# Kernel tuning notes

Hardware: AMD Instinct MI355X
Metric: run time of the kernel (lower is better)

The kernel has to match this reference:

```python
import jax, jax.numpy as jnp
import numpy as np

NUM_CLASSES = 3
EXCEPT_THRESH = 0.05
NMS_THRESH = 0.5
NMS_TOPK = 500
BATCH = 16
ANCHORS_PER_LOC = 3


def _make_scale(key, grid, stride):
    """Build realistic YOLO-style output / anchor / offset / stride tensors for one scale."""
    A = ANCHORS_PER_LOC
    N = grid * grid * A
    out = jax.random.normal(key, (BATCH, N, 5 + NUM_CLASSES), dtype=jnp.float32)
    ys, xs = jnp.meshgrid(jnp.arange(grid, dtype=jnp.float32),
                          jnp.arange(grid, dtype=jnp.float32), indexing='ij')
    off = jnp.stack([xs, ys], axis=-1).reshape(grid * grid, 1, 2)         # (G*G,1,2)
    off = jnp.broadcast_to(off, (grid * grid, A, 2)).reshape(1, N, 2)
    base = jnp.array([[16., 16.], [32., 24.], [24., 48.]], jnp.float32) * (stride / 8.0)
    anc = jnp.broadcast_to(base.reshape(1, 1, A, 2), (1, grid * grid, A, 2)).reshape(1, N, 2)
    st = jnp.full((1, 1, 2), stride, dtype=jnp.float32)
    return out, anc, off, st


def setup_inputs() -> dict:
    key = jax.random.key(0)
    k1, k2, k3 = jax.random.split(key, 3)
    o1, a1, f1, s1 = _make_scale(k1, 96, 8.0)
    o2, a2, f2, s2 = _make_scale(k2, 48, 16.0)
    o3, a3, f3, s3 = _make_scale(k3, 24, 32.0)
    return {
        'output1': o1, 'output2': o2, 'output3': o3,
        'anchor1': a1, 'anchor2': a2, 'anchor3': a3,
        'offset1': f1, 'offset2': f2, 'offset3': f3,
        'stride1': s1, 'stride2': s2, 'stride3': s3,
    }


def _decode(out, anchor, offset, stride):
    """YOLOv3 multiperclass decode -> (B, N*C, 6) rows of [id, score, x1, y1, x2, y2]."""
    xy, wh = out[..., 0:2], out[..., 2:4]
    obj, cls = out[..., 4:5], out[..., 5:]
    # from_sigmoid=False: apply sigmoid to centers / objectness / class logits
    xy = jax.nn.sigmoid(xy)
    obj = jax.nn.sigmoid(obj)
    cls = jax.nn.sigmoid(cls)
    center = (xy + offset) * stride              # (B,N,2)
    half = 0.5 * jnp.exp(wh) * anchor            # (B,N,2)
    bbox = jnp.concatenate([center - half, center + half], axis=-1)  # (B,N,4)
    scores = obj * cls                           # (B,N,C)
    B, N, C = scores.shape
    ids = jnp.broadcast_to(jnp.arange(C, dtype=jnp.float32), (B, N, C))
    mask = scores > EXCEPT_THRESH
    ids = jnp.where(mask, ids, -1.0)
    scr = jnp.where(mask, scores, -1.0)
    bb = jnp.broadcast_to(bbox[:, :, None, :], (B, N, C, 4))
    res = jnp.concatenate([ids[..., None], scr[..., None], bb], axis=-1)
    return res.reshape(B, N * C, 6)


def _iou_matrix(boxes):
    """boxes (K,4) corner format -> (K,K) IoU."""
    x1, y1, x2, y2 = boxes[:, 0], boxes[:, 1], boxes[:, 2], boxes[:, 3]
    area = jnp.maximum(x2 - x1, 0.0) * jnp.maximum(y2 - y1, 0.0)
    iw = jnp.maximum(jnp.minimum(x2[:, None], x2[None]) - jnp.maximum(x1[:, None], x1[None]), 0.0)
    ih = jnp.maximum(jnp.minimum(y2[:, None], y2[None]) - jnp.maximum(y1[:, None], y1[None]), 0.0)
    inter = iw * ih
    return inter / (area[:, None] + area[None] - inter + 1e-12)


def _greedy_keep(iou, valid):
    """Greedy NMS over score-sorted candidates. iou (K,K), valid (K,) -> keep (K,) bool."""
    K = iou.shape[0]
    ar = jnp.arange(K)
    def body(i, keep):
        suppressed = jnp.any(keep & (ar < i) & (iou[i] > NMS_THRESH))
        return keep.at[i].set(valid[i] & ~suppressed)
    return jax.lax.fori_loop(0, K, body, valid)


def _per_class_nms(ids, scores, bboxes):
    """ids/scores (B,M,1), bboxes (B,M,4). Suppressed candidates get id=-1, score=-1.
    uid=-1 (background / below-threshold) entries pass through untouched, matching the
    original which skips NMS for uid<0."""
    B, M = ids.shape[:2]
    idf, scf = ids[..., 0], scores[..., 0]
    scatter = jax.vmap(lambda kf, o, k: kf.at[o].set(k))
    for c in range(NUM_CLASSES):
        cmask = idf == float(c)
        s = jnp.where(cmask, scf, -jnp.inf)
        order = jnp.argsort(-s, axis=1)[:, :NMS_TOPK]            # (B,K)
        sb = jnp.take_along_axis(s, order, axis=1)               # (B,K)
        bb = jnp.take_along_axis(bboxes, order[..., None], axis=1)  # (B,K,4)
        valid = jnp.isfinite(sb)
        iou = jax.vmap(_iou_matrix)(bb)                          # (B,K,K)
        keep = jax.vmap(_greedy_keep)(iou, valid)                # (B,K)
        keep_full = scatter(jnp.zeros((B, M), bool), order, keep)
        sup = cmask & ~keep_full                                 # suppressed or beyond topk
        idf = jnp.where(sup, -1.0, idf)
        scf = jnp.where(sup, -1.0, scf)
    return idf[..., None], scf[..., None], bboxes


def reference(output1, output2, output3, anchor1, anchor2, anchor3,
              offset1, offset2, offset3, stride1, stride2, stride3):
    results = jnp.concatenate([
        _decode(output1, anchor1, offset1, stride1),
        _decode(output2, anchor2, offset2, stride2),
        _decode(output3, anchor3, offset3, stride3),
    ], axis=1)                                   # (B, M, 6)
    ids = results[:, :, 0:1]
    scores = results[:, :, 1:2]
    bboxes = results[:, :, 2:]
    return _per_class_nms(ids, scores, bboxes)
```

## Files before the change

kernel.cpp:

```cpp
#include <hip/hip_runtime.h>

#define N1 27648
#define N2 6912
#define N3 1728
#define NTOT 36288
#define BATCH_ 16
#define C_ 3
#define GRP (BATCH_ * C_)
#define MROWS (NTOT * C_)
#define TOPK 500
#define NBINS 2304
#define CCAP 2048
#define BASEBITS 0x3D400000u
#define TPRE 0.5f
#define LISTCAP 4096
#define CNT_STRIDE 32

#define OFF_LIST   8192ull
#define SZ_LIST    ((size_t)GRP * LISTCAP * 8)
#define OFF_KEYS   (OFF_LIST + SZ_LIST)
#define SZ_KEYS    ((size_t)GRP * 512 * 8)
#define OFF_BOXES  (OFF_KEYS + SZ_KEYS)
#define SZ_BOXES   ((size_t)GRP * 512 * 16)
#define OFF_MASKS  (OFF_BOXES + SZ_BOXES)
#define SZ_MASKS   ((size_t)GRP * 4096 * 8)
#define OFF_KCNT   (OFF_MASKS + SZ_MASKS)
#define SZ_KCNT    4096ull
#define WS_NEED    (OFF_KCNT + SZ_KCNT)

__device__ __forceinline__ float sigm(float x) { return 1.0f / (1.0f + expf(-x)); }

__device__ __forceinline__ float score_of(int b, int n, int c,
    const float* __restrict__ o1, const float* __restrict__ o2, const float* __restrict__ o3)
{
    const float* o; int ln, Ns;
    if (n < N1)           { o = o1; ln = n;             Ns = N1; }
    else if (n < N1 + N2) { o = o2; ln = n - N1;        Ns = N2; }
    else                  { o = o3; ln = n - (N1 + N2); Ns = N3; }
    const float* r = o + ((size_t)b * Ns + ln) * 8;
    return sigm(r[4]) * sigm(r[5 + c]);
}

__device__ __forceinline__ unsigned wave_push(bool pred, unsigned* cntp)
{
    unsigned long long mb = __ballot(pred);
    unsigned pos = 0xFFFFFFFFu;
    if (pred) {
        int lane = threadIdx.x & 63;
        int leader = __ffsll((long long)mb) - 1;
        unsigned total = (unsigned)__popcll(mb);
        unsigned base = 0;
        if (lane == leader) base = atomicAdd(cntp, total);
        base = __shfl(base, leader);
        pos = base + (unsigned)__popcll(mb & ((1ull << lane) - 1ull));
    }
    return pos;
}

__device__ __forceinline__ void scan_tb(const unsigned* hist, unsigned* sh_tb)
{
    const int tid = threadIdx.x;
    if (tid < 64) {
        const int CHUNK = NBINS / 64;
        int base_i = tid * CHUNK;
        unsigned own = 0;
        #pragma unroll
        for (int k = 0; k < CHUNK; ++k) own += hist[base_i + k];
        unsigned sfx = own;
        #pragma unroll
        for (int off = 1; off < 64; off <<= 1) {
            unsigned v = __shfl_down(sfx, off, 64);
            sfx += (tid + off < 64) ? v : 0u;
        }
        unsigned sfxn = sfx - own;
        if (tid == 0 && sfx < TOPK) *sh_tb = 0u;
        if (sfx >= TOPK && sfxn < TOPK) {
            unsigned cum = sfxn, tb = (unsigned)base_i;
            for (int k = CHUNK - 1; k >= 0; --k) {
                cum += hist[base_i + k];
                if (cum >= TOPK) { tb = (unsigned)(base_i + k); break; }
            }
            *sh_tb = tb;
        }
    }
}

__global__ __launch_bounds__(64) void zerocnt_kernel(unsigned* __restrict__ cnts)
{
    if (threadIdx.x < GRP) cnts[threadIdx.x * CNT_STRIDE] = 0u;
}

__global__ __launch_bounds__(256) void decode_filter_kernel(
    const float* __restrict__ o1, const float* __restrict__ o2, const float* __restrict__ o3,
    const float* __restrict__ a1, const float* __restrict__ a2, const float* __restrict__ a3,
    const float* __restrict__ f1, const float* __restrict__ f2, const float* __restrict__ f3,
    const float* __restrict__ s1, const float* __restrict__ s2, const float* __restrict__ s3,
    float* __restrict__ out,
    unsigned* __restrict__ cnts, unsigned long long* __restrict__ list, int listcap)
{
    __shared__ unsigned lcnt[C_];
    __shared__ unsigned lbase[C_];
    __shared__ unsigned long long stage[C_][256];

    const int tid = threadIdx.x;
    const int n = blockIdx.x * 256 + tid;
    const int b = blockIdx.y;

    if (tid < C_) lcnt[tid] = 0u;
    __syncthreads();

    if (n < NTOT) {
        const float *o, *anc, *off, *st; int ln, Ns;
        if (n < N1)           { o = o1; anc = a1; off = f1; st = s1; ln = n;             Ns = N1; }
        else if (n < N1 + N2) { o = o2; anc = a2; off = f2; st = s2; ln = n - N1;        Ns = N2; }
        else                  { o = o3; anc = a3; off = f3; st = s3; ln = n - (N1 + N2); Ns = N3; }
        const float* r = o + ((size_t)b * Ns + ln) * 8;
        float4 v0 = *(const float4*)r;
        float4 v1 = *(const float4*)(r + 4);

        float sx = sigm(v0.x);
        float sy = sigm(v0.y);
        float cx = (sx + off[2 * ln + 0]) * st[0];
        float cy = (sy + off[2 * ln + 1]) * st[1];
        float hx = 0.5f * expf(v0.z) * anc[2 * ln + 0];
        float hy = 0.5f * expf(v0.w) * anc[2 * ln + 1];
        float4 bb = make_float4(cx - hx, cy - hy, cx + hx, cy + hy);

        size_t base = (size_t)b * MROWS + (size_t)n * C_;
        float* ids = out;
        float* scs = out + (size_t)BATCH_ * MROWS;
        float* bbs = out + 2ull * BATCH_ * MROWS;

        __builtin_nontemporal_store(-1.0f, &ids[base + 0]);
        __builtin_nontemporal_store(-1.0f, &ids[base + 1]);
        __builtin_nontemporal_store(-1.0f, &ids[base + 2]);
        __builtin_nontemporal_store(-1.0f, &scs[base + 0]);
        __builtin_nontemporal_store(-1.0f, &scs[base + 1]);
        __builtin_nontemporal_store(-1.0f, &scs[base + 2]);
        float4* bp = (float4*)(bbs + base * 4);
        bp[0] = bb; bp[1] = bb; bp[2] = bb;

        if (listcap > 0) {
            float sobj = sigm(v1.x);
            float s[3] = { sobj * sigm(v1.y), sobj * sigm(v1.z), sobj * sigm(v1.w) };
            #pragma unroll
            for (int c = 0; c < C_; ++c) {
                if (s[c] > TPRE) {
                    unsigned p = atomicAdd(&lcnt[c], 1u);
                    stage[c][p] =
                        ((unsigned long long)__float_as_uint(s[c]) << 32) | (unsigned)(~n);
                }
            }
        }
    }

    if (listcap > 0) {
        __syncthreads();
        if (tid < C_)
            lbase[tid] = atomicAdd(&cnts[(b * C_ + tid) * CNT_STRIDE], lcnt[tid]);
        __syncthreads();
        #pragma unroll
        for (int c = 0; c < C_; ++c) {
            unsigned m = lcnt[c];
            if ((unsigned)tid < m) {
                unsigned pos = lbase[c] + (unsigned)tid;
                if (pos < (unsigned)listcap)
                    list[(size_t)(b * C_ + c) * listcap + pos] = stage[c][tid];
            }
        }
    }
}

__global__ __launch_bounds__(512) void topk_kernel(
    const float* __restrict__ o1, const float* __restrict__ o2, const float* __restrict__ o3,
    const float* __restrict__ out,
    const unsigned* __restrict__ cnts, const unsigned long long* __restrict__ list,
    unsigned long long* __restrict__ gkeys, float4* __restrict__ gboxes,
    unsigned* __restrict__ kcnt)
{
    const int g = blockIdx.x;
    const int b = g / C_;
    const int c = g - b * C_;
    const int tid = threadIdx.x;

    __shared__ unsigned long long smem[CCAP + 1152];
    unsigned long long* keys = smem;
    unsigned* hist = (unsigned*)(smem + CCAP);
    unsigned long long* skeys = smem + CCAP;
    __shared__ unsigned int sh_tb, sh_cnt;

    unsigned cnt_g = cnts[g * CNT_STRIDE];
    const bool pathL = (cnt_g >= TOPK && cnt_g <= (unsigned)LISTCAP);
    const unsigned long long* L = list + (size_t)g * LISTCAP;

    for (int i = tid; i < NBINS; i += 512) hist[i] = 0u;
    if (tid == 0) sh_cnt = 0u;
    __syncthreads();

    if (pathL) {
        #pragma unroll 4
        for (unsigned i = tid; i < cnt_g; i += 512) {
            unsigned bin = ((unsigned)(L[i] >> 32) - BASEBITS) >> 14;
            if (bin > NBINS - 1u) bin = NBINS - 1u;
            atomicAdd(&hist[bin], 1u);
        }
    } else {
        for (int n = tid; n < NTOT; n += 512) {
            float s = score_of(b, n, c, o1, o2, o3);
            if (s > 0.05f) {
                unsigned bin = (__float_as_uint(s) - BASEBITS) >> 14;
                if (bin > NBINS - 1u) bin = NBINS - 1u;
                atomicAdd(&hist[bin], 1u);
            }
        }
    }
    __syncthreads();

    scan_tb(hist, &sh_tb);
    __syncthreads();

    const unsigned tb = sh_tb;
    if (pathL) {
        unsigned nIter = (cnt_g + 511u) & ~511u;
        #pragma unroll 4
        for (unsigned i = tid; i < nIter; i += 512) {
            bool pred = false; unsigned long long key = 0ull;
            if (i < cnt_g) {
                key = L[i];
                unsigned bin = ((unsigned)(key >> 32) - BASEBITS) >> 14;
                if (bin > NBINS - 1u) bin = NBINS - 1u;
                pred = (bin >= tb);
            }
            unsigned p = wave_push(pred, &sh_cnt);
            if (pred && p < CCAP) keys[p] = key;
        }
    } else {
        const int nIter = (NTOT + 511) & ~511;
        for (int n = tid; n < nIter; n += 512) {
            bool pred = false; unsigned long long key = 0ull;
            if (n < NTOT) {
                float s = score_of(b, n, c, o1, o2, o3);
                if (s > 0.05f) {
                    unsigned bits = __float_as_uint(s);
                    unsigned bin = (bits - BASEBITS) >> 14;
                    if (bin > NBINS - 1u) bin = NBINS - 1u;
                    if (bin >= tb) {
                        pred = true;
                        key = ((unsigned long long)bits << 32) | (unsigned)(~n);
                    }
                }
            }
            unsigned p = wave_push(pred, &sh_cnt);
            if (pred && p < CCAP) keys[p] = key;
        }
    }
    __syncthreads();

    const unsigned cnt2 = min(sh_cnt, (unsigned)CCAP);
    const int K = (int)min(cnt2, (unsigned)TOPK);

    for (unsigned m = tid; m < cnt2; m += 512) {
        unsigned long long km = keys[m];
        unsigned rank = 0;
        #pragma unroll 4
        for (unsigned j = 0; j < cnt2; ++j)
            rank += (keys[j] > km) ? 1u : 0u;
        if (rank < 512u) skeys[rank] = km;
    }
    __syncthreads();

    if (tid == 0) kcnt[g] = (unsigned)K;
    if (tid < K) {
        unsigned long long key = skeys[tid];
        gkeys[(size_t)g * 512 + tid] = key;
        unsigned idx = ~(unsigned)(key & 0xFFFFFFFFull);
        const float* bbs = out + 2ull * BATCH_ * MROWS;
        gboxes[(size_t)g * 512 + tid] =
            *(const float4*)(bbs + ((size_t)b * MROWS + (size_t)idx * C_) * 4);
    }
}

__global__ __launch_bounds__(256) void masks_kernel(
    const float4* __restrict__ gboxes, const unsigned* __restrict__ kcnt,
    unsigned long long* __restrict__ gmasks)
{
    const int g = blockIdx.x;
    const int w = blockIdx.y;
    const int K = (int)kcnt[g];

    __shared__ float bx[TOPK * 4];
    __shared__ float ar[TOPK];

    const float4* B = gboxes + (size_t)g * 512;
    for (int j = threadIdx.x; j < K; j += 256) {
        float4 v = B[j];
        bx[j*4+0] = v.x; bx[j*4+1] = v.y; bx[j*4+2] = v.z; bx[j*4+3] = v.w;
        ar[j] = fmaxf(v.z - v.x, 0.0f) * fmaxf(v.w - v.y, 0.0f);
    }
    __syncthreads();

    unsigned long long* M = gmasks + (size_t)g * 4096 + (size_t)w * 512;
    const int j0 = w * 64;
    const int jhi = (K < j0 + 64) ? K : j0 + 64;

    for (int i = threadIdx.x; i < K; i += 256) {
        unsigned long long word = 0ull;
        if (i + 1 < jhi) {
            float xi1 = bx[i*4+0], yi1 = bx[i*4+1], xi2 = bx[i*4+2], yi2 = bx[i*4+3];
            float ai = ar[i];
            for (int j = j0; j < jhi; ++j) {
                float xj1 = bx[j*4+0], yj1 = bx[j*4+1], xj2 = bx[j*4+2], yj2 = bx[j*4+3];
                float aj = ar[j];
                float iw = fmaxf(fminf(xi2, xj2) - fmaxf(xi1, xj1), 0.0f);
                float ih = fmaxf(fminf(yi2, yj2) - fmaxf(yi1, yj1), 0.0f);
                float inter = iw * ih;
                float iou = inter / (ai + aj - inter + 1e-12f);
                if (iou > 0.5f && j > i) word |= 1ull << (j - j0);
            }
        }
        M[i] = word;
    }
}

__global__ __launch_bounds__(512) void greedy_kernel(
    const unsigned long long* __restrict__ gmasks,
    const unsigned long long* __restrict__ gkeys,
    const unsigned* __restrict__ kcnt, float* __restrict__ out)
{
    const int g = blockIdx.x;
    const int b = g / C_;
    const int c = g - b * C_;
    const int tid = threadIdx.x;
    const int K = (int)kcnt[g];

    __shared__ unsigned long long mlds[512 * 9];
    __shared__ unsigned long long keep_s[8];

    const unsigned long long* GM = gmasks + (size_t)g * 4096;
    for (int t = tid; t < 8 * 512; t += 512) {
        int w = t >> 9, i = t & 511;
        mlds[i * 9 + w] = (i < K) ? GM[w * 512 + i] : 0ull;
    }
    __syncthreads();

    if (tid < 64) {
        const int lane8 = tid & 7;
        unsigned long long removed = 0ull, keep = 0ull;
        const int Kpad = (K + 7) & ~7;

        unsigned long long m0 = mlds[0*9+lane8], m1 = mlds[1*9+lane8],
                           m2 = mlds[2*9+lane8], m3 = mlds[3*9+lane8],
                           m4 = mlds[4*9+lane8], m5 = mlds[5*9+lane8],
                           m6 = mlds[6*9+lane8], m7 = mlds[7*9+lane8];

        for (int i0 = 0; i0 < Kpad; i0 += 8) {
            int nb = (i0 + 8 < 512) ? (i0 + 8) : 0;
            unsigned long long n0 = mlds[(nb+0)*9+lane8], n1 = mlds[(nb+1)*9+lane8],
                               n2 = mlds[(nb+2)*9+lane8], n3 = mlds[(nb+3)*9+lane8],
                               n4 = mlds[(nb+4)*9+lane8], n5 = mlds[(nb+5)*9+lane8],
                               n6 = mlds[(nb+6)*9+lane8], n7 = mlds[(nb+7)*9+lane8];

            #define GSTEP(t, mt) { \
                int i = i0 + t; \
                int w = i >> 6, bp = i & 63; \
                bool mine = (tid == w) && ((removed >> bp) & 1ull); \
                unsigned long long alive = __any(mine) ? 0ull : ~0ull; \
                keep |= ((tid == w) ? (1ull << bp) : 0ull) & alive; \
                removed |= mt & alive; \
            }
            GSTEP(0, m0) GSTEP(1, m1) GSTEP(2, m2) GSTEP(3, m3)
            GSTEP(4, m4) GSTEP(5, m5) GSTEP(6, m6) GSTEP(7, m7)
            #undef GSTEP

            m0=n0; m1=n1; m2=n2; m3=n3; m4=n4; m5=n5; m6=n6; m7=n7;
        }
        if (tid < 8) keep_s[tid] = keep;
    }
    __syncthreads();

    const unsigned long long* GK = gkeys + (size_t)g * 512;
    for (int i = tid; i < K; i += 512) {
        if ((keep_s[i >> 6] >> (i & 63)) & 1ull) {
            unsigned long long key = GK[i];
            unsigned idx = ~(unsigned)(key & 0xFFFFFFFFull);
            float sc = __uint_as_float((unsigned)(key >> 32));
            size_t row = (size_t)b * MROWS + (size_t)idx * C_ + c;
            out[row] = (float)c;
            out[(size_t)BATCH_ * MROWS + row] = sc;
        }
    }
}

__global__ __launch_bounds__(512) void select_nms_mono(
    const float* __restrict__ o1, const float* __restrict__ o2, const float* __restrict__ o3,
    float* __restrict__ out)
{
    const int g = blockIdx.x;
    const int b = g / C_;
    const int c = g - b * C_;
    const int tid = threadIdx.x;

    __shared__ unsigned long long smem[7048];
    __shared__ unsigned int sh_tb, sh_cnt;
    __shared__ unsigned long long keepw[8];

    unsigned long long* keys = smem;
    unsigned* hist = (unsigned*)(smem + CCAP);
    unsigned long long* skeys = smem + CCAP;
    float* boxes = (float*)(smem + CCAP + 600);
    unsigned long long* masks = smem + 3048;

    for (int i = tid; i < NBINS; i += 512) hist[i] = 0u;
    if (tid == 0) sh_cnt = 0u;
    __syncthreads();

    for (int n = tid; n < NTOT; n += 512) {
        float s = score_of(b, n, c, o1, o2, o3);
        if (s > 0.05f) {
            unsigned bin = (__float_as_uint(s) - BASEBITS) >> 14;
            if (bin > NBINS - 1u) bin = NBINS - 1u;
            atomicAdd(&hist[bin], 1u);
        }
    }
    __syncthreads();
    scan_tb(hist, &sh_tb);
    __syncthreads();

    const unsigned tb = sh_tb;
    for (int n = tid; n < NTOT; n += 512) {
        float s = score_of(b, n, c, o1, o2, o3);
        if (s > 0.05f) {
            unsigned bits = __float_as_uint(s);
            unsigned bin = (bits - BASEBITS) >> 14;
            if (bin > NBINS - 1u) bin = NBINS - 1u;
            if (bin >= tb) {
                unsigned p = atomicAdd(&sh_cnt, 1u);
                if (p < CCAP)
                    keys[p] = ((unsigned long long)bits << 32) | (unsigned)(~n);
            }
        }
    }
    __syncthreads();

    const unsigned cnt2 = min(sh_cnt, (unsigned)CCAP);
    const int K = (int)min(cnt2, (unsigned)TOPK);

    for (unsigned m = tid; m < cnt2; m += 512) {
        unsigned long long km = keys[m];
        unsigned rank = 0;
        for (unsigned j = 0; j < cnt2; ++j)
            rank += (keys[j] > km) ? 1u : 0u;
        if (rank < 512u) skeys[rank] = km;
    }
    __syncthreads();
    if (tid < K) keys[tid] = skeys[tid];
    __syncthreads();

    {
        const float* bbs = out + 2ull * BATCH_ * MROWS;
        if (tid < K) {
            unsigned idx = ~(unsigned)(keys[tid] & 0xFFFFFFFFull);
            float4 bb = *(const float4*)(bbs + ((size_t)b * MROWS + (size_t)idx * C_) * 4);
            ((float4*)boxes)[tid] = bb;
        }
    }
    __syncthreads();

    {
        const int nw = (K + 63) >> 6;
        for (int t = tid; t < K * nw; t += 512) {
            int w = t / K;
            int i = t - w * K;
            float xi1 = boxes[i*4+0], yi1 = boxes[i*4+1], xi2 = boxes[i*4+2], yi2 = boxes[i*4+3];
            float ai = fmaxf(xi2 - xi1, 0.0f) * fmaxf(yi2 - yi1, 0.0f);
            unsigned long long word = 0ull;
            int jlo = (i + 1 > w * 64) ? i + 1 : w * 64;
            int jhi = (K < (w + 1) * 64) ? K : (w + 1) * 64;
            for (int j = jlo; j < jhi; ++j) {
                float xj1 = boxes[j*4+0], yj1 = boxes[j*4+1], xj2 = boxes[j*4+2], yj2 = boxes[j*4+3];
                float aj = fmaxf(xj2 - xj1, 0.0f) * fmaxf(yj2 - yj1, 0.0f);
                float iw = fmaxf(fminf(xi2, xj2) - fmaxf(xi1, xj1), 0.0f);
                float ih = fmaxf(fminf(yi2, yj2) - fmaxf(yi1, yj1), 0.0f);
                float inter = iw * ih;
                float iou = inter / (ai + aj - inter + 1e-12f);
                if (iou > 0.5f) word |= 1ull << (j & 63);
            }
            masks[i * 8 + w] = word;
        }
    }
    __syncthreads();

    if (tid < 64) {
        unsigned long long removed = 0ull, keep = 0ull;
        for (int i = 0; i < K; ++i) {
            unsigned long long mw = (tid < 8) ? masks[i * 8 + tid] : 0ull;
            int w = i >> 6, bp = i & 63;
            bool mine = (tid == w) && ((removed >> bp) & 1ull);
            if (!__any(mine)) {
                if (tid == w) keep |= 1ull << bp;
                removed |= mw;
            }
        }
        if (tid < 8) keepw[tid] = keep;
    }
    __syncthreads();

    if (tid < K && ((keepw[tid >> 6] >> (tid & 63)) & 1ull)) {
        unsigned long long key = keys[tid];
        unsigned idx = ~(unsigned)(key & 0xFFFFFFFFull);
        float sc = __uint_as_float((unsigned)(key >> 32));
        size_t row = (size_t)b * MROWS + (size_t)idx * C_ + c;
        out[row] = (float)c;
        out[(size_t)BATCH_ * MROWS + row] = sc;
    }
}

extern "C" void kernel_launch(void* const* d_in, const int* in_sizes, int n_in,
                              void* d_out, int out_size, void* d_ws, size_t ws_size,
                              hipStream_t stream)
{
    const float* o1 = (const float*)d_in[0];
    const float* o2 = (const float*)d_in[1];
    const float* o3 = (const float*)d_in[2];
    const float* a1 = (const float*)d_in[3];
    const float* a2 = (const float*)d_in[4];
    const float* a3 = (const float*)d_in[5];
    const float* f1 = (const float*)d_in[6];
    const float* f2 = (const float*)d_in[7];
    const float* f3 = (const float*)d_in[8];
    const float* s1 = (const float*)d_in[9];
    const float* s2 = (const float*)d_in[10];
    const float* s3 = (const float*)d_in[11];
    float* out = (float*)d_out;

    unsigned* cnts = (unsigned*)d_ws;

    if (ws_size >= WS_NEED) {
        unsigned long long* list   = (unsigned long long*)((char*)d_ws + OFF_LIST);
        unsigned long long* gkeys  = (unsigned long long*)((char*)d_ws + OFF_KEYS);
        float4*             gboxes = (float4*)((char*)d_ws + OFF_BOXES);
        unsigned long long* gmasks = (unsigned long long*)((char*)d_ws + OFF_MASKS);
        unsigned*           kcnt   = (unsigned*)((char*)d_ws + OFF_KCNT);

        zerocnt_kernel<<<dim3(1), dim3(64), 0, stream>>>(cnts);
        decode_filter_kernel<<<dim3((NTOT + 255) / 256, BATCH_), dim3(256), 0, stream>>>(
            o1, o2, o3, a1, a2, a3, f1, f2, f3, s1, s2, s3, out, cnts, list, LISTCAP);
        topk_kernel<<<dim3(GRP), dim3(512), 0, stream>>>(
            o1, o2, o3, out, cnts, list, gkeys, gboxes, kcnt);
        masks_kernel<<<dim3(GRP, 8), dim3(256), 0, stream>>>(gboxes, kcnt, gmasks);
        greedy_kernel<<<dim3(GRP), dim3(512), 0, stream>>>(gmasks, gkeys, kcnt, out);
    } else {
        decode_filter_kernel<<<dim3((NTOT + 255) / 256, BATCH_), dim3(256), 0, stream>>>(
            o1, o2, o3, a1, a2, a3, f1, f2, f3, s1, s2, s3, out, nullptr, nullptr, 0);
        select_nms_mono<<<dim3(GRP), dim3(512), 0, stream>>>(o1, o2, o3, out);
    }
}
```

Measured before the change: 94.20 us.

## Fuse decode, top-k, mask and greedy NMS stages into one cooperative kernel

Replaces the five separate launches (zero counters, decode/filter, top-k, IoU masks, greedy) with a single cooperative mega-kernel of 256 blocks that separates the stages with grid-wide syncs. The aim is to remove per-launch overhead and inter-kernel gaps. In exchange, the decode stage runs on far fewer blocks with grid-stride loops, and grid.sync barriers plus thread fences add their own cost. It falls back to the old multi-kernel path if cooperative launch is unsupported or fails.

Measured after the change: 315.7 us. 235% more time.

```diff
diff --git a/kernel.cpp b/kernel.cpp
--- a/kernel.cpp
+++ b/kernel.cpp
@@ -1,4 +1,7 @@
 #include <hip/hip_runtime.h>
+#include <hip/hip_cooperative_groups.h>
+
+namespace cg = cooperative_groups;
 
 #define N1 27648
 #define N2 6912
@@ -28,6 +31,8 @@
 #define SZ_KCNT    4096ull
 #define WS_NEED    (OFF_KCNT + SZ_KCNT)
 
+#define COOP_BLOCKS 256
+
 __device__ __forceinline__ float sigm(float x) { return 1.0f / (1.0f + expf(-x)); }
 
 __device__ __forceinline__ float score_of(int b, int n, int c,
@@ -85,6 +90,304 @@
     }
 }
 
+__global__ __launch_bounds__(512) void mega_kernel(
+    const float* __restrict__ o1, const float* __restrict__ o2, const float* __restrict__ o3,
+    const float* __restrict__ a1, const float* __restrict__ a2, const float* __restrict__ a3,
+    const float* __restrict__ f1, const float* __restrict__ f2, const float* __restrict__ f3,
+    const float* __restrict__ s1, const float* __restrict__ s2, const float* __restrict__ s3,
+    float* __restrict__ out,
+    unsigned* __restrict__ cnts, unsigned long long* __restrict__ list,
+    unsigned long long* __restrict__ gkeys, float4* __restrict__ gboxes,
+    unsigned long long* __restrict__ gmasks, unsigned* __restrict__ kcnt)
+{
+    cg::grid_group gg = cg::this_grid();
+    const int bid = blockIdx.x;
+    const int tid = threadIdx.x;
+
+    __shared__ unsigned long long smem[4616];
+    __shared__ unsigned lcnt[C_], lbase[C_];
+    __shared__ unsigned sh_tb, sh_cnt;
+    __shared__ unsigned long long keep_s[8];
+
+    if (bid == 0 && tid < GRP) cnts[tid * CNT_STRIDE] = 0u;
+    gg.sync();
+
+    {
+        unsigned long long (*stage)[512] = (unsigned long long (*)[512])smem;
+        const int TPB = (NTOT + 511) / 512;
+        for (int t = bid; t < TPB * BATCH_; t += gridDim.x) {
+            const int b = t / TPB;
+            const int x = t - b * TPB;
+            const int n = x * 512 + tid;
+            if (tid < C_) lcnt[tid] = 0u;
+            __syncthreads();
+            if (n < NTOT) {
+                const float *o, *anc, *off, *st; int ln, Ns;
+                if (n < N1)           { o = o1; anc = a1; off = f1; st = s1; ln = n;             Ns = N1; }
+                else if (n < N1 + N2) { o = o2; anc = a2; off = f2; st = s2; ln = n - N1;        Ns = N2; }
+                else                  { o = o3; anc = a3; off = f3; st = s3; ln = n - (N1 + N2); Ns = N3; }
+                const float* r = o + ((size_t)b * Ns + ln) * 8;
+                float4 v0 = *(const float4*)r;
+                float4 v1 = *(const float4*)(r + 4);
+
+                float sx = sigm(v0.x);
+                float sy = sigm(v0.y);
+                float cx = (sx + off[2 * ln + 0]) * st[0];
+                float cy = (sy + off[2 * ln + 1]) * st[1];
+                float hx = 0.5f * expf(v0.z) * anc[2 * ln + 0];
+                float hy = 0.5f * expf(v0.w) * anc[2 * ln + 1];
+                float4 bb = make_float4(cx - hx, cy - hy, cx + hx, cy + hy);
+
+                size_t base = (size_t)b * MROWS + (size_t)n * C_;
+                float* ids = out;
+                float* scs = out + (size_t)BATCH_ * MROWS;
+                float* bbs = out + 2ull * BATCH_ * MROWS;
+
+                __builtin_nontemporal_store(-1.0f, &ids[base + 0]);
+                __builtin_nontemporal_store(-1.0f, &ids[base + 1]);
+                __builtin_nontemporal_store(-1.0f, &ids[base + 2]);
+                __builtin_nontemporal_store(-1.0f, &scs[base + 0]);
+                __builtin_nontemporal_store(-1.0f, &scs[base + 1]);
+                __builtin_nontemporal_store(-1.0f, &scs[base + 2]);
+                float4* bp = (float4*)(bbs + base * 4);
+                bp[0] = bb; bp[1] = bb; bp[2] = bb;
+
+                float sobj = sigm(v1.x);
+                float s[3] = { sobj * sigm(v1.y), sobj * sigm(v1.z), sobj * sigm(v1.w) };
+                #pragma unroll
+                for (int c = 0; c < C_; ++c) {
+                    if (s[c] > TPRE) {
+                        unsigned p = atomicAdd(&lcnt[c], 1u);
+                        stage[c][p] =
+                            ((unsigned long long)__float_as_uint(s[c]) << 32) | (unsigned)(~n);
+                    }
+                }
+            }
+            __syncthreads();
+            if (tid < C_)
+                lbase[tid] = atomicAdd(&cnts[(b * C_ + tid) * CNT_STRIDE], lcnt[tid]);
+            __syncthreads();
+            #pragma unroll
+            for (int c = 0; c < C_; ++c) {
+                unsigned m = lcnt[c];
+                if ((unsigned)tid < m) {
+                    unsigned pos = lbase[c] + (unsigned)tid;
+                    if (pos < (unsigned)LISTCAP)
+                        list[(size_t)(b * C_ + c) * LISTCAP + pos] = stage[c][tid];
+                }
+            }
+            __syncthreads();
+        }
+    }
+    __threadfence();
+    gg.sync();
+
+    if (bid < GRP) {
+        const int g = bid;
+        const int b = g / C_;
+        const int c = g - b * C_;
+
+        unsigned long long* keys = smem;
+        unsigned* hist = (unsigned*)(smem + CCAP);
+        unsigned long long* skeys = smem + CCAP;
+
+        unsigned cnt_g = cnts[g * CNT_STRIDE];
+        const bool pathL = (cnt_g >= TOPK && cnt_g <= (unsigned)LISTCAP);
+        const unsigned long long* L = list + (size_t)g * LISTCAP;
+
+        for (int i = tid; i < NBINS; i += 512) hist[i] = 0u;
+        if (tid == 0) sh_cnt = 0u;
+        __syncthreads();
+
+        if (pathL) {
+            #pragma unroll 4
+            for (unsigned i = tid; i < cnt_g; i += 512) {
+                unsigned bin = ((unsigned)(L[i] >> 32) - BASEBITS) >> 14;
+                if (bin > NBINS - 1u) bin = NBINS - 1u;
+                atomicAdd(&hist[bin], 1u);
+            }
+        } else {
+            for (int n = tid; n < NTOT; n += 512) {
+                float s = score_of(b, n, c, o1, o2, o3);
+                if (s > 0.05f) {
+                    unsigned bin = (__float_as_uint(s) - BASEBITS) >> 14;
+                    if (bin > NBINS - 1u) bin = NBINS - 1u;
+                    atomicAdd(&hist[bin], 1u);
+                }
+            }
+        }
+        __syncthreads();
+        scan_tb(hist, &sh_tb);
+        __syncthreads();
+
+        const unsigned tb = sh_tb;
+        if (pathL) {
+            unsigned nIter = (cnt_g + 511u) & ~511u;
+            #pragma unroll 4
+            for (unsigned i = tid; i < nIter; i += 512) {
+                bool pred = false; unsigned long long key = 0ull;
+                if (i < cnt_g) {
+                    key = L[i];
+                    unsigned bin = ((unsigned)(key >> 32) - BASEBITS) >> 14;
+                    if (bin > NBINS - 1u) bin = NBINS - 1u;
+                    pred = (bin >= tb);
+                }
+                unsigned p = wave_push(pred, &sh_cnt);
+                if (pred && p < CCAP) keys[p] = key;
+            }
+        } else {
+            const int nIter = (NTOT + 511) & ~511;
+            for (int n = tid; n < nIter; n += 512) {
+                bool pred = false; unsigned long long key = 0ull;
+                if (n < NTOT) {
+                    float s = score_of(b, n, c, o1, o2, o3);
+                    if (s > 0.05f) {
+                        unsigned bits = __float_as_uint(s);
+                        unsigned bin = (bits - BASEBITS) >> 14;
+                        if (bin > NBINS - 1u) bin = NBINS - 1u;
+                        if (bin >= tb) {
+                            pred = true;
+                            key = ((unsigned long long)bits << 32) | (unsigned)(~n);
+                        }
+                    }
+                }
+                unsigned p = wave_push(pred, &sh_cnt);
+                if (pred && p < CCAP) keys[p] = key;
+            }
+        }
+        __syncthreads();
+
+        const unsigned cnt2 = min(sh_cnt, (unsigned)CCAP);
+        const int K = (int)min(cnt2, (unsigned)TOPK);
+
+        for (unsigned m = tid; m < cnt2; m += 512) {
+            unsigned long long km = keys[m];
+            unsigned rank = 0;
+            #pragma unroll 4
+            for (unsigned j = 0; j < cnt2; ++j)
+                rank += (keys[j] > km) ? 1u : 0u;
+            if (rank < 512u) skeys[rank] = km;
+        }
+        __syncthreads();
+
+        if (tid == 0) kcnt[g] = (unsigned)K;
+        if (tid < K) {
+            unsigned long long key = skeys[tid];
+            gkeys[(size_t)g * 512 + tid] = key;
+            unsigned idx = ~(unsigned)(key & 0xFFFFFFFFull);
+            const float* bbs = out + 2ull * BATCH_ * MROWS;
+            gboxes[(size_t)g * 512 + tid] =
+                *(const float4*)(bbs + ((size_t)b * MROWS + (size_t)idx * C_) * 4);
+        }
+    }
+    __threadfence();
+    gg.sync();
+
+    {
+        float* bx = (float*)smem;
+        float* ar = (float*)(smem + 1000);
+        for (int task = bid; task < GRP * 8; task += gridDim.x) {
+            const int g = task >> 3;
+            const int w = task & 7;
+            const int K = (int)kcnt[g];
+            __syncthreads();
+            const float4* B = gboxes + (size_t)g * 512;
+            for (int j = tid; j < K; j += 512) {
+                float4 v = B[j];
+                bx[j*4+0] = v.x; bx[j*4+1] = v.y; bx[j*4+2] = v.z; bx[j*4+3] = v.w;
+                ar[j] = fmaxf(v.z - v.x, 0.0f) * fmaxf(v.w - v.y, 0.0f);
+            }
+            __syncthreads();
+
+            unsigned long long* M = gmasks + (size_t)g * 4096 + (size_t)w * 512;
+            const int j0 = w * 64;
+            const int jhi = (K < j0 + 64) ? K : j0 + 64;
+            for (int i = tid; i < K; i += 512) {
+                unsigned long long word = 0ull;
+                if (i + 1 < jhi) {
+                    float xi1 = bx[i*4+0], yi1 = bx[i*4+1], xi2 = bx[i*4+2], yi2 = bx[i*4+3];
+                    float ai = ar[i];
+                    for (int j = j0; j < jhi; ++j) {
+                        float xj1 = bx[j*4+0], yj1 = bx[j*4+1], xj2 = bx[j*4+2], yj2 = bx[j*4+3];
+                        float aj = ar[j];
+                        float iw = fmaxf(fminf(xi2, xj2) - fmaxf(xi1, xj1), 0.0f);
+                        float ih = fmaxf(fminf(yi2, yj2) - fmaxf(yi1, yj1), 0.0f);
+                        float inter = iw * ih;
+                        float iou = inter / (ai + aj - inter + 1e-12f);
+                        if (iou > 0.5f && j > i) word |= 1ull << (j - j0);
+                    }
+                }
+                M[i] = word;
+            }
+        }
+    }
+    __threadfence();
+    gg.sync();
+
+    if (bid < GRP) {
+        const int g = bid;
+        const int b = g / C_;
+        const int c = g - b * C_;
+        const int K = (int)kcnt[g];
+
+        unsigned long long* mlds = smem;
+        const unsigned long long* GM = gmasks + (size_t)g * 4096;
+        for (int t = tid; t < 8 * 512; t += 512) {
+            int w = t >> 9, i = t & 511;
+            mlds[i * 9 + w] = (i < K) ? GM[w * 512 + i] : 0ull;
+        }
+        __syncthreads();
+
+        if (tid < 64) {
+            const int lane8 = tid & 7;
+            unsigned long long removed = 0ull, keep = 0ull;
+            const int Kpad = (K + 7) & ~7;
+
+            unsigned long long m0 = mlds[0*9+lane8], m1 = mlds[1*9+lane8],
+                               m2 = mlds[2*9+lane8], m3 = mlds[3*9+lane8],
+                               m4 = mlds[4*9+lane8], m5 = mlds[5*9+lane8],
+                               m6 = mlds[6*9+lane8], m7 = mlds[7*9+lane8];
+
+            for (int i0 = 0; i0 < Kpad; i0 += 8) {
+                int nb = (i0 + 8 < 512) ? (i0 + 8) : 0;
+                unsigned long long n0 = mlds[(nb+0)*9+lane8], n1 = mlds[(nb+1)*9+lane8],
+                                   n2 = mlds[(nb+2)*9+lane8], n3 = mlds[(nb+3)*9+lane8],
+                                   n4 = mlds[(nb+4)*9+lane8], n5 = mlds[(nb+5)*9+lane8],
+                                   n6 = mlds[(nb+6)*9+lane8], n7 = mlds[(nb+7)*9+lane8];
+
+                #define GSTEP(t, mt) { \
+                    int i = i0 + t; \
+                    int w = i >> 6, bp = i & 63; \
+                    bool mine = (tid == w) && ((removed >> bp) & 1ull); \
+                    unsigned long long alive = __any(mine) ? 0ull : ~0ull; \
+                    keep |= ((tid == w) ? (1ull << bp) : 0ull) & alive; \
+                    removed |= mt & alive; \
+                }
+                GSTEP(0, m0) GSTEP(1, m1) GSTEP(2, m2) GSTEP(3, m3)
+                GSTEP(4, m4) GSTEP(5, m5) GSTEP(6, m6) GSTEP(7, m7)
+                #undef GSTEP
+
+                m0=n0; m1=n1; m2=n2; m3=n3; m4=n4; m5=n5; m6=n6; m7=n7;
+            }
+            if (tid < 8) keep_s[tid] = keep;
+        }
+        __syncthreads();
+
+        const unsigned long long* GK = gkeys + (size_t)g * 512;
+        for (int i = tid; i < K; i += 512) {
+            if ((keep_s[i >> 6] >> (i & 63)) & 1ull) {
+                unsigned long long key = GK[i];
+                unsigned idx = ~(unsigned)(key & 0xFFFFFFFFull);
+                float sc = __uint_as_float((unsigned)(key >> 32));
+                size_t row = (size_t)b * MROWS + (size_t)idx * C_ + c;
+                out[row] = (float)c;
+                out[(size_t)BATCH_ * MROWS + row] = sc;
+            }
+        }
+    }
+}
+
+
 __global__ __launch_bounds__(64) void zerocnt_kernel(unsigned* __restrict__ cnts)
 {
     if (threadIdx.x < GRP) cnts[threadIdx.x * CNT_STRIDE] = 0u;
@@ -215,7 +518,6 @@
         }
     }
     __syncthreads();
-
     scan_tb(hist, &sh_tb);
     __syncthreads();
 
@@ -533,14 +835,32 @@
     const float* s3 = (const float*)d_in[11];
     float* out = (float*)d_out;
 
-    unsigned* cnts = (unsigned*)d_ws;
-
     if (ws_size >= WS_NEED) {
+        unsigned*           cnts   = (unsigned*)d_ws;
         unsigned long long* list   = (unsigned long long*)((char*)d_ws + OFF_LIST);
         unsigned long long* gkeys  = (unsigned long long*)((char*)d_ws + OFF_KEYS);
         float4*             gboxes = (float4*)((char*)d_ws + OFF_BOXES);
         unsigned long long* gmasks = (unsigned long long*)((char*)d_ws + OFF_MASKS);
         unsigned*           kcnt   = (unsigned*)((char*)d_ws + OFF_KCNT);
+
+        int dev = 0;
+        (void)hipGetDevice(&dev);
+        int coop = 0;
+        (void)hipDeviceGetAttribute(&coop, hipDeviceAttributeCooperativeLaunch, dev);
+
+        if (coop) {
+            void* args[] = { (void*)&o1, (void*)&o2, (void*)&o3,
+                             (void*)&a1, (void*)&a2, (void*)&a3,
+                             (void*)&f1, (void*)&f2, (void*)&f3,
+                             (void*)&s1, (void*)&s2, (void*)&s3,
+                             (void*)&out, (void*)&cnts, (void*)&list,
+                             (void*)&gkeys, (void*)&gboxes, (void*)&gmasks, (void*)&kcnt };
+            hipError_t err = hipLaunchCooperativeKernel(
+                reinterpret_cast<const void*>(mega_kernel),
+                dim3(COOP_BLOCKS), dim3(512), args, 0, stream);
+            if (err == hipSuccess) return;
+            (void)hipGetLastError();
+        }
 
         zerocnt_kernel<<<dim3(1), dim3(64), 0, stream>>>(cnts);
         decode_filter_kernel<<<dim3((NTOT + 255) / 256, BATCH_), dim3(256), 0, stream>>>(
```
